# Kernel optimization log

Hardware: AMD Instinct MI355X
Metric: run time of the kernel (lower is better)

The kernel has to match this reference:

```python
import jax, jax.numpy as jnp
import numpy as np

KERNEL_SIZE = 65
STRIDE = 1
PAD = (KERNEL_SIZE - 1) // 2  # padding='same'


def setup_inputs() -> dict:
    key = jax.random.key(0)
    k1, k2 = jax.random.split(key)
    B, Cin, T = 8, 512, 512
    out_size = (Cin + 2 * PAD - (KERNEL_SIZE - 1) - 1) // STRIDE + 1  # 512
    x = jax.random.normal(k1, (B, Cin, T), dtype=jnp.float32)
    # per-output-position weights, init randn/sqrt(K) as in the torch module
    weights = jax.random.normal(k2, (out_size, 1, KERNEL_SIZE), dtype=jnp.float32) / jnp.sqrt(
        jnp.float32(KERNEL_SIZE)
    )
    bias = jnp.zeros((out_size, 1), dtype=jnp.float32)
    return {"x": x, "weights": weights, "bias": bias}


def reference(x, weights, bias):
    # x: (B, Cin, T) -> output (B, T, out_size)
    out_size, _, K = weights.shape
    xt = jnp.swapaxes(x, 1, 2)                       # (B, T, Cin)
    xp = jnp.pad(xt, ((0, 0), (0, 0), (PAD, PAD)))   # (B, T, Cin + 2p)
    # sliding windows over the (padded) channel axis: (out_size, K) gather indices
    idx = jnp.arange(out_size)[:, None] * STRIDE + jnp.arange(K)[None, :]
    win = xp[:, :, idx]                              # (B, T, out_size, K)
    # locally-connected matvec: distinct K-vector per output position o
    y = jnp.einsum("btok,ok->bto", win, weights[:, 0, :])
    y = y + bias[:, 0]                               # (B, T, out_size)
    return y
```

## Files before the change

### kernel.cpp

```cpp
#include <hip/hip_runtime.h>

#define B_    8
#define C_    512
#define T_    512
#define O_    512
#define K_    65
#define PAD_  32

#define O_TILE 32
#define T_TILE 128
#define J_     8
#define NW     4
#define ROWS   (O_TILE + 2 * PAD_)
#define NR     (J_ + 2 * PAD_)
#define YPITCH 36

#define XTILE_ELEMS (ROWS * T_TILE)
#define WT_TILE     (NW * NR * J_)

__global__ __launch_bounds__(256, 2)
void conv_fused(const float* __restrict__ x,
                const float* __restrict__ w,
                const float* __restrict__ bias,
                float* __restrict__ out) {
    __shared__ float smem[XTILE_ELEMS + WT_TILE];
    float* xs  = smem;
    float* wts = smem + XTILE_ELEMS;

    const int tid = threadIdx.x;
    const int bid = blockIdx.x;
    const int b   = bid >> 6;
    const int rem = bid & 63;
    const int ob  = rem >> 2;
    const int tb  = rem & 3;
    const int t0  = tb * T_TILE;
    const int c_base = ob * O_TILE - PAD_;

    {
        const float* xb = x + (size_t)b * (C_ * T_);
        const int l32 = tid & 31;
        const int rg  = tid >> 5;
        #pragma unroll
        for (int rr = 0; rr < ROWS / 8; ++rr) {
            const int row = rr * 8 + rg;
            const int c   = c_base + row;
            float4 v = make_float4(0.f, 0.f, 0.f, 0.f);
            if (c >= 0 && c < C_)
                v = *(const float4*)(xb + c * T_ + t0 + l32 * 4);
            *(float4*)(&xs[row * T_TILE + l32 * 4]) = v;
        }
    }

    {
        #pragma unroll
        for (int p = 0; p < WT_TILE / 256; ++p) {
            const int e  = p * 256 + tid;
            const int wg = e / (NR * J_);
            const int r2 = e % (NR * J_);
            const int r  = r2 >> 3;
            const int j  = r2 & 7;
            const int o  = (ob * NW + wg) * J_ + j;
            const int k  = r - j;
            float v = 0.f;
            if (k >= 0 && k < K_) v = w[o * K_ + k];
            wts[e] = v;
        }
    }
    __syncthreads();

    const int lane  = tid & 63;
    const int wu    = __builtin_amdgcn_readfirstlane(tid >> 6);
    const int obase = (ob * NW + wu) * J_;

    float2 acc[J_];
    #pragma unroll
    for (int j = 0; j < J_; ++j) {
        const float bj = bias[obase + j];
        acc[j] = make_float2(bj, bj);
    }

    const int tl = lane * 2;
    const float* xrow = xs + (wu * J_) * T_TILE + tl;
    const float* wrow = wts + wu * (NR * J_);

    #pragma unroll 4
    for (int r = 0; r < NR; ++r) {
        const float2 xv = *(const float2*)(xrow + r * T_TILE);
        const float4 wa = *(const float4*)(wrow + r * J_);
        const float4 wb = *(const float4*)(wrow + r * J_ + 4);
        acc[0].x += wa.x * xv.x;  acc[0].y += wa.x * xv.y;
        acc[1].x += wa.y * xv.x;  acc[1].y += wa.y * xv.y;
        acc[2].x += wa.z * xv.x;  acc[2].y += wa.z * xv.y;
        acc[3].x += wa.w * xv.x;  acc[3].y += wa.w * xv.y;
        acc[4].x += wb.x * xv.x;  acc[4].y += wb.x * xv.y;
        acc[5].x += wb.y * xv.x;  acc[5].y += wb.y * xv.y;
        acc[6].x += wb.z * xv.x;  acc[6].y += wb.z * xv.y;
        acc[7].x += wb.w * xv.x;  acc[7].y += wb.w * xv.y;
    }

    __syncthreads();

    {
        const int olb = wu * J_;
        *(float4*)(&smem[tl * YPITCH + olb])           = make_float4(acc[0].x, acc[1].x, acc[2].x, acc[3].x);
        *(float4*)(&smem[tl * YPITCH + olb + 4])       = make_float4(acc[4].x, acc[5].x, acc[6].x, acc[7].x);
        *(float4*)(&smem[(tl + 1) * YPITCH + olb])     = make_float4(acc[0].y, acc[1].y, acc[2].y, acc[3].y);
        *(float4*)(&smem[(tl + 1) * YPITCH + olb + 4]) = make_float4(acc[4].y, acc[5].y, acc[6].y, acc[7].y);
    }
    __syncthreads();

    {
        float* ob_out = out + (size_t)b * (T_ * O_) + (size_t)t0 * O_ + ob * O_TILE;
        const int ol   = (tid & 7) * 4;
        const int trow = tid >> 3;
        #pragma unroll
        for (int p = 0; p < 4; ++p) {
            const int t_local = p * 32 + trow;
            const float4 v = *(const float4*)(&smem[t_local * YPITCH + ol]);
            *(float4*)(ob_out + (size_t)t_local * O_ + ol) = v;
        }
    }
}

extern "C" void kernel_launch(void* const* d_in, const int* in_sizes, int n_in,
                              void* d_out, int out_size, void* d_ws, size_t ws_size,
                              hipStream_t stream) {
    const float* x    = (const float*)d_in[0];
    const float* w    = (const float*)d_in[1];
    const float* bias = (const float*)d_in[2];
    float* out = (float*)d_out;

    const int nblocks = B_ * (O_ / O_TILE) * (T_ / T_TILE);
    conv_fused<<<nblocks, 256, 0, stream>>>(x, w, bias, out);
}
```

Measured before the change: 75.54 us.

## Precompute banded weight layout in workspace and read weights from global memory

Adds a small prep kernel that expands the per-output weights into the banded (r, j) layout once per call in workspace. The main kernel then reads weights directly from global or L2 through wave-uniform float4 loads instead of building the band in shared memory in every block. This removes the per-block weight staging and its index arithmetic, and shrinks shared memory. The cost is an extra kernel launch and global loads inside the inner loop. The loop unroll also goes from 4 to 8.

```diff
diff --git a/kernel.cpp b/kernel.cpp
--- a/kernel.cpp
+++ b/kernel.cpp
@@ -17,15 +17,32 @@
 
 #define XTILE_ELEMS (ROWS * T_TILE)
 #define WT_TILE     (NW * NR * J_)
+#define NOG        (O_ / J_)
+#define WT_ELEMS   (NOG * NR * J_)
 
+__global__ __launch_bounds__(256) void wt_prep(const float* __restrict__ w,
+                                               float* __restrict__ wt) {
+    int e = blockIdx.x * 256 + threadIdx.x;
+    if (e >= WT_ELEMS) return;
+    int og  = e / (NR * J_);
+    int rem = e % (NR * J_);
+    int r   = rem >> 3;
+    int j   = rem & 7;
+    int k   = r - j;
+    float v = 0.0f;
+    if (k >= 0 && k < K_) v = w[(og * J_ + j) * K_ + k];
+    wt[e] = v;
+}
+
+template <bool USE_WS>
 __global__ __launch_bounds__(256, 2)
-void conv_fused(const float* __restrict__ x,
-                const float* __restrict__ w,
-                const float* __restrict__ bias,
-                float* __restrict__ out) {
-    __shared__ float smem[XTILE_ELEMS + WT_TILE];
-    float* xs  = smem;
-    float* wts = smem + XTILE_ELEMS;
+void conv_main(const float* __restrict__ x,
+               const float* __restrict__ w,
+               const float* __restrict__ wt,
+               const float* __restrict__ bias,
+               float* __restrict__ out) {
+    __shared__ float smem[XTILE_ELEMS + (USE_WS ? 0 : WT_TILE)];
+    float* xs = smem;
 
     const int tid = threadIdx.x;
     const int bid = blockIdx.x;
@@ -51,7 +68,8 @@
         }
     }
 
-    {
+    if (!USE_WS) {
+        float* wts = smem + XTILE_ELEMS;
         #pragma unroll
         for (int p = 0; p < WT_TILE / 256; ++p) {
             const int e  = p * 256 + tid;
@@ -70,7 +88,8 @@
 
     const int lane  = tid & 63;
     const int wu    = __builtin_amdgcn_readfirstlane(tid >> 6);
-    const int obase = (ob * NW + wu) * J_;
+    const int og    = ob * NW + wu;
+    const int obase = og * J_;
 
     float2 acc[J_];
     #pragma unroll
@@ -81,13 +100,15 @@
 
     const int tl = lane * 2;
     const float* xrow = xs + (wu * J_) * T_TILE + tl;
-    const float* wrow = wts + wu * (NR * J_);
+    const float4* wrow = USE_WS
+        ? (const float4*)(wt + (size_t)og * (NR * J_))
+        : (const float4*)(smem + XTILE_ELEMS + wu * (NR * J_));
 
-    #pragma unroll 4
+    #pragma unroll 8
     for (int r = 0; r < NR; ++r) {
         const float2 xv = *(const float2*)(xrow + r * T_TILE);
-        const float4 wa = *(const float4*)(wrow + r * J_);
-        const float4 wb = *(const float4*)(wrow + r * J_ + 4);
+        const float4 wa = wrow[2 * r];
+        const float4 wb = wrow[2 * r + 1];
         acc[0].x += wa.x * xv.x;  acc[0].y += wa.x * xv.y;
         acc[1].x += wa.y * xv.x;  acc[1].y += wa.y * xv.y;
         acc[2].x += wa.z * xv.x;  acc[2].y += wa.z * xv.y;
@@ -129,7 +150,14 @@
     const float* w    = (const float*)d_in[1];
     const float* bias = (const float*)d_in[2];
     float* out = (float*)d_out;
+    float* wt  = (float*)d_ws;
 
     const int nblocks = B_ * (O_ / O_TILE) * (T_ / T_TILE);
-    conv_fused<<<nblocks, 256, 0, stream>>>(x, w, bias, out);
+
+    if (ws_size >= (size_t)WT_ELEMS * sizeof(float)) {
+        wt_prep<<<(WT_ELEMS + 255) / 256, 256, 0, stream>>>(w, wt);
+        conv_main<true><<<nblocks, 256, 0, stream>>>(x, w, wt, bias, out);
+    } else {
+        conv_main<false><<<nblocks, 256, 0, stream>>>(x, w, w, bias, out);
+    }
 }
```

Result: no change. 74.53 us (-1.3%).
